# Performance work log

Hardware: AMD Instinct MI355X
Metric: run time of the kernel (lower is better)

The kernel has to match this reference:

```python
import jax, jax.numpy as jnp
import numpy as np

D_MODEL = 512
NHEAD = 8
D_K = D_MODEL // NHEAD


def setup_inputs() -> dict:
    key = jax.random.key(0)
    ks = jax.random.split(key, 9)
    s = 1.0 / np.sqrt(D_MODEL)
    x = jax.random.normal(ks[0], (2, 2048, D_MODEL), dtype=jnp.float32)
    # torch Linear weights: [out_features, in_features]
    Wq = jax.random.uniform(ks[1], (D_MODEL, D_MODEL), jnp.float32, -s, s)
    bq = jax.random.uniform(ks[2], (D_MODEL,), jnp.float32, -s, s)
    Wk = jax.random.uniform(ks[3], (D_MODEL, D_MODEL), jnp.float32, -s, s)
    bk = jax.random.uniform(ks[4], (D_MODEL,), jnp.float32, -s, s)
    Wv = jax.random.uniform(ks[5], (D_MODEL, D_MODEL), jnp.float32, -s, s)
    bv = jax.random.uniform(ks[6], (D_MODEL,), jnp.float32, -s, s)
    Wo = jax.random.uniform(ks[7], (D_MODEL, D_MODEL), jnp.float32, -s, s)
    bo = jax.random.uniform(ks[8], (D_MODEL,), jnp.float32, -s, s)
    return {"x": x, "Wq": Wq, "bq": bq, "Wk": Wk, "bk": bk,
            "Wv": Wv, "bv": bv, "Wo": Wo, "bo": bo}


def reference(x, Wq, bq, Wk, bk, Wv, bv, Wo, bo):
    B, S, D = x.shape
    H, Dk = NHEAD, D_K

    def proj(W, b):
        # torch Linear: x @ W.T + b -> [B, S, D] -> [B, H, S, Dk]
        y = jnp.einsum('bsd,ed->bse', x, W) + b
        return y.reshape(B, S, H, Dk).transpose(0, 2, 1, 3)

    q = proj(Wq, bq)
    k = proj(Wk, bk)
    v = proj(Wv, bv)

    scores = jnp.einsum('bhqd,bhkd->bhqk', q, k) / jnp.sqrt(jnp.float32(Dk))
    attn = jax.nn.softmax(scores, axis=-1)  # explicit O(S^2) attention matrix
    out = jnp.einsum('bhqk,bhkd->bhqd', attn, v)
    out = out.transpose(0, 2, 1, 3).reshape(B, S, D)
    return jnp.einsum('bsd,ed->bse', out, Wo) + bo
```

## Files before the change

### kernel.cpp

```cpp
#include <hip/hip_runtime.h>

typedef __bf16 bf16_t;
typedef bf16_t bf16x8 __attribute__((ext_vector_type(8)));
typedef bf16_t bf16x4 __attribute__((ext_vector_type(4)));
typedef float  floatx4 __attribute__((ext_vector_type(4)));
typedef short  s16x4   __attribute__((ext_vector_type(4)));

#define D_MODEL 512
#define NHEAD   8
#define DK      64
#define BATCH   2
#define SEQ     2048
#define MTOT    (BATCH*SEQ)
#define QSCALE  0.18033688011112042591f

static __device__ __forceinline__ floatx4 mfma16(bf16x8 a, bf16x8 b, floatx4 c) {
    return __builtin_amdgcn_mfma_f32_16x16x32_bf16(a, b, c, 0, 0, 0);
}
static __device__ __forceinline__ floatx4 mfma16k16(s16x4 a, s16x4 b, floatx4 c) {
    return __builtin_amdgcn_mfma_f32_16x16x16bf16_1k(a, b, c, 0, 0, 0);
}

static __device__ __forceinline__ void glds16(bf16_t* lds, const bf16_t* g) {
    __builtin_amdgcn_global_load_lds(
        (const __attribute__((address_space(1))) unsigned int*)g,
        (__attribute__((address_space(3))) unsigned int*)lds,
        16, 0, 0);
}

__global__ __launch_bounds__(256)
void to_bf16(const float* __restrict__ x,
             const float* __restrict__ Wq, const float* __restrict__ Wk,
             const float* __restrict__ Wv, const float* __restrict__ Wo,
             bf16_t* __restrict__ xb, bf16_t* __restrict__ wqb,
             bf16_t* __restrict__ wkb, bf16_t* __restrict__ wvb,
             bf16_t* __restrict__ wob)
{
    const int blk = blockIdx.x;
    const float* src; bf16_t* dst; size_t base;
    if      (blk < 1024) { src = x;  dst = xb;  base = (size_t)blk * 2048; }
    else if (blk < 1152) { src = Wq; dst = wqb; base = (size_t)(blk - 1024) * 2048; }
    else if (blk < 1280) { src = Wk; dst = wkb; base = (size_t)(blk - 1152) * 2048; }
    else if (blk < 1408) { src = Wv; dst = wvb; base = (size_t)(blk - 1280) * 2048; }
    else                 { src = Wo; dst = wob; base = (size_t)(blk - 1408) * 2048; }
    const size_t off = base + (size_t)threadIdx.x * 8;
    const float4 a = *(const float4*)(src + off);
    const float4 b = *(const float4*)(src + off + 4);
    bf16x8 p;
    p[0]=(bf16_t)a.x; p[1]=(bf16_t)a.y; p[2]=(bf16_t)a.z; p[3]=(bf16_t)a.w;
    p[4]=(bf16_t)b.x; p[5]=(bf16_t)b.y; p[6]=(bf16_t)b.z; p[7]=(bf16_t)b.w;
    const size_t off2 = off ^ ((((off >> 10) & 3)) << 3);
    *(bf16x8*)(dst + off2) = p;
}

__global__ __launch_bounds__(256)
void qkv_proj(const bf16_t* __restrict__ xb,
              const bf16_t* __restrict__ wqb, const float* __restrict__ bq,
              const bf16_t* __restrict__ wkb, const float* __restrict__ bk,
              const bf16_t* __restrict__ wvb, const float* __restrict__ bv,
              bf16_t* __restrict__ q_ws, bf16_t* __restrict__ k_ws,
              bf16_t* __restrict__ vt_ws)
{
    __shared__ bf16_t As[128 * 32];
    __shared__ bf16_t Bs[128 * 32];

    const int mtile = blockIdx.x;
    const int ntile = blockIdx.y;
    const int which = ntile >> 2;
    const int nsub  = ntile & 3;
    const bf16_t* W   = (which == 0) ? wqb : (which == 1) ? wkb : wvb;
    const float* bias = (which == 0) ? bq  : (which == 1) ? bk  : bv;

    const int tid  = threadIdx.x;
    const int lane = tid & 63;
    const int wave = tid >> 6;
    const int wm = wave & 1, wn = wave >> 1;
    const int l15 = lane & 15, quad = lane >> 4;
    const int m0 = mtile * 128;
    const int n0 = nsub * 128;
    const int lr = lane >> 2;
    const int lc = (lane & 3) * 8;
    const int csw = (quad ^ ((l15 >> 1) & 3)) * 8;

    floatx4 acc[4][4] = {};

    for (int k0 = 0; k0 < 512; k0 += 32) {
        __syncthreads();
        #pragma unroll
        for (int q = 0; q < 2; ++q) {
            const int r = wave * 32 + q * 16;
            glds16(&As[r * 32], xb + (size_t)(m0 + r + lr) * 512 + k0 + lc);
            glds16(&Bs[r * 32], W  + (size_t)(n0 + r + lr) * 512 + k0 + lc);
        }
        __syncthreads();

        bf16x8 af[4], bfr[4];
        #pragma unroll
        for (int i = 0; i < 4; ++i)
            af[i] = *(const bf16x8*)(&As[(wm * 64 + i * 16 + l15) * 32 + csw]);
        #pragma unroll
        for (int j = 0; j < 4; ++j)
            bfr[j] = *(const bf16x8*)(&Bs[(wn * 64 + j * 16 + l15) * 32 + csw]);
        #pragma unroll
        for (int i = 0; i < 4; ++i)
            #pragma unroll
            for (int j = 0; j < 4; ++j)
                acc[i][j] = mfma16(af[i], bfr[j], acc[i][j]);
    }

    #pragma unroll
    for (int j = 0; j < 4; ++j) {
        const int e = n0 + wn * 64 + j * 16 + l15;
        const float be = bias[e];
        const int h = e >> 6, d = e & 63;
        #pragma unroll
        for (int i = 0; i < 4; ++i) {
            const int mbase = m0 + wm * 64 + i * 16 + quad * 4;
            const int b = mbase >> 11;
            const int sl = mbase & 2047;
            floatx4 c = acc[i][j];
            if (which == 2) {
                bf16x4 pk;
                #pragma unroll
                for (int r = 0; r < 4; ++r) pk[r] = (bf16_t)(c[r] + be);
                const int slz = (sl & ~63) | ((((sl >> 3) & 7) ^ (d & 7)) << 3) | (sl & 7);
                *(bf16x4*)(vt_ws + ((size_t)((b * 8 + h) * 64 + d)) * 2048 + slz) = pk;
            } else if (which == 1) {
                #pragma unroll
                for (int r = 0; r < 4; ++r) {
                    const int s = sl + r;
                    const int dz = ((((d >> 3) ^ (s & 7))) << 3) | (d & 7);
                    k_ws[(size_t)(b * 8 + h) * (SEQ * DK) + (size_t)s * 64 + dz] =
                        (bf16_t)(c[r] + be);
                }
            } else {
                #pragma unroll
                for (int r = 0; r < 4; ++r)
                    q_ws[(size_t)(b * 8 + h) * (SEQ * DK) + (size_t)(sl + r) * 64 + d] =
                        (bf16_t)((c[r] + be) * QSCALE);
            }
        }
    }
}

__global__ __launch_bounds__(256, 4)
void attn_kernel(const bf16_t* __restrict__ q_ws, const bf16_t* __restrict__ k_ws,
                 const bf16_t* __restrict__ vt_ws, bf16_t* __restrict__ attn_ws)
{
    __shared__ bf16_t Kt[2][64 * 64];
    __shared__ bf16_t Vt[2][64 * 64];

    const int bh = blockIdx.x;
    const int qt = blockIdx.y;
    const int tid = threadIdx.x, lane = tid & 63, wave = tid >> 6;
    const int l15 = lane & 15, quad = lane >> 4;
    const int g  = wave >> 1;
    const int wq = wave & 1;

    const bf16_t* Qb  = q_ws  + (size_t)bh * SEQ * DK;
    const bf16_t* Kb  = k_ws  + (size_t)bh * SEQ * DK;
    const bf16_t* Vtb = vt_ws + (size_t)bh * DK * SEQ;

    const int sp = wave & 1;
    bf16_t* stile = (wave < 2) ? &Kt[sp][0] : &Vt[sp][0];
    const int srow8 = lane >> 3;
    const int scol  = (lane & 7) * 8;

    bf16x8 aq[2][2];
    #pragma unroll
    for (int mt = 0; mt < 2; ++mt)
        #pragma unroll
        for (int c = 0; c < 2; ++c)
            aq[mt][c] = *(const bf16x8*)(Qb +
                (size_t)(qt * 64 + wq * 32 + mt * 16 + l15) * 64 + c * 32 + quad * 8);

    floatx4 O[2][4] = {};
    float rs[2] = {0.f, 0.f};
    const int ksw0 = ((0 + quad) ^ (l15 & 7)) * 8;
    const int ksw1 = ((4 + quad) ^ (l15 & 7)) * 8;

    for (int t = 0; t < 16; ++t) {
        __syncthreads();
        {
            const int kg = t * 128 + sp * 64;
            if (wave < 2) {
                #pragma unroll
                for (int i = 0; i < 8; ++i)
                    glds16(stile + i * 512,
                           Kb + (size_t)(kg + i * 8 + srow8) * 64 + scol);
            } else {
                #pragma unroll
                for (int i = 0; i < 8; ++i)
                    glds16(stile + i * 512,
                           Vtb + (size_t)(i * 8 + srow8) * 2048 + kg + scol);
            }
        }
        __syncthreads();

        s16x4 pf[2][4];
        #pragma unroll
        for (int kf = 0; kf < 4; ++kf) {
            const bf16_t* krow = &Kt[g][(kf * 16 + l15) * 64];
            bf16x8 k0 = *(const bf16x8*)(krow + ksw0);
            bf16x8 k1 = *(const bf16x8*)(krow + ksw1);
            #pragma unroll
            for (int mt = 0; mt < 2; ++mt) {
                floatx4 z = {0.f, 0.f, 0.f, 0.f};
                z = mfma16(k0, aq[mt][0], z);
                z = mfma16(k1, aq[mt][1], z);
                bf16x4 pk;
                float s = 0.f;
                #pragma unroll
                for (int r = 0; r < 4; ++r) {
                    const float p = __builtin_amdgcn_exp2f(z[r]);
                    s += p;
                    pk[r] = (bf16_t)p;
                }
                rs[mt] += s;
                pf[mt][kf] = __builtin_bit_cast(s16x4, pk);
            }
        }

        #pragma unroll
        for (int kg = 0; kg < 4; ++kg) {
            const int voff = (((kg * 2 + (quad >> 1)) ^ (l15 & 7)) * 8) + (quad & 1) * 4;
            #pragma unroll
            for (int df = 0; df < 4; ++df) {
                const s16x4 v = *(const s16x4*)(&Vt[g][(df * 16 + l15) * 64 + voff]);
                #pragma unroll
                for (int mt = 0; mt < 2; ++mt)
                    O[mt][df] = mfma16k16(pf[mt][kg], v, O[mt][df]);
            }
        }
    }

    #pragma unroll
    for (int mt = 0; mt < 2; ++mt) {
        rs[mt] += __shfl_xor(rs[mt], 16, 64);
        rs[mt] += __shfl_xor(rs[mt], 32, 64);
    }

    float* scratch = (float*)&Kt[0][0];
    __syncthreads();
    if (g == 1) {
        float* s = scratch + (size_t)(wq * 64 + lane) * 35;
        #pragma unroll
        for (int mt = 0; mt < 2; ++mt) {
            #pragma unroll
            for (int df = 0; df < 4; ++df)
                #pragma unroll
                for (int r = 0; r < 4; ++r) s[mt * 16 + df * 4 + r] = O[mt][df][r];
            s[32 + mt] = rs[mt];
        }
    }
    __syncthreads();
    if (g == 0) {
        const float* s = scratch + (size_t)(wq * 64 + lane) * 35;
        #pragma unroll
        for (int mt = 0; mt < 2; ++mt) {
            #pragma unroll
            for (int df = 0; df < 4; ++df)
                #pragma unroll
                for (int r = 0; r < 4; ++r) O[mt][df][r] += s[mt * 16 + df * 4 + r];
            rs[mt] += s[32 + mt];
        }

        const int b = bh >> 3, h = bh & 7;
        #pragma unroll
        for (int mt = 0; mt < 2; ++mt)
            #pragma unroll
            for (int r = 0; r < 4; ++r) {
                const float rv = __shfl(rs[mt], (quad << 4) + ((quad & 3) << 2) + r, 64);
                const float rinv = 1.0f / rv;
                const int s_ = qt * 64 + wq * 32 + mt * 16 + quad * 4 + r;
                const int sw = ((s_ >> 1) & 3) << 3;
                const size_t base = ((size_t)b * 2048 + s_) * 512;
                #pragma unroll
                for (int df = 0; df < 4; ++df) {
                    const int col = h * 64 + df * 16 + l15;
                    attn_ws[base + (col ^ sw)] = (bf16_t)(O[mt][df][r] * rinv);
                }
            }
    }
}

__global__ __launch_bounds__(256)
void out_proj(const bf16_t* __restrict__ attn_ws, const bf16_t* __restrict__ wob,
              const float* __restrict__ bo, float* __restrict__ y)
{
    __shared__ bf16_t As[64 * 32];
    __shared__ bf16_t Bs[128 * 32];

    const int mtile = blockIdx.x;
    const int ntile = blockIdx.y;
    const int tid = threadIdx.x, lane = tid & 63, wave = tid >> 6;
    const int wm = wave & 1, wn = wave >> 1;
    const int l15 = lane & 15, quad = lane >> 4;
    const int m0 = mtile * 64;
    const int n0 = ntile * 128;
    const int lr = lane >> 2, lc = (lane & 3) * 8;
    const int csw = (quad ^ ((l15 >> 1) & 3)) * 8;

    floatx4 acc[2][4] = {};

    for (int k0 = 0; k0 < 512; k0 += 32) {
        __syncthreads();
        glds16(&As[wave * 16 * 32], attn_ws + (size_t)(m0 + wave * 16 + lr) * 512 + k0 + lc);
        #pragma unroll
        for (int q = 0; q < 2; ++q) {
            const int r = wave * 32 + q * 16;
            glds16(&Bs[r * 32], wob + (size_t)(n0 + r + lr) * 512 + k0 + lc);
        }
        __syncthreads();

        bf16x8 af[2], bfr[4];
        #pragma unroll
        for (int i = 0; i < 2; ++i)
            af[i] = *(const bf16x8*)(&As[(wm * 32 + i * 16 + l15) * 32 + csw]);
        #pragma unroll
        for (int j = 0; j < 4; ++j)
            bfr[j] = *(const bf16x8*)(&Bs[(wn * 64 + j * 16 + l15) * 32 + csw]);
        #pragma unroll
        for (int i = 0; i < 2; ++i)
            #pragma unroll
            for (int j = 0; j < 4; ++j)
                acc[i][j] = mfma16(af[i], bfr[j], acc[i][j]);
    }

    #pragma unroll
    for (int j = 0; j < 4; ++j) {
        const int e = n0 + wn * 64 + j * 16 + l15;
        const float be = bo[e];
        #pragma unroll
        for (int i = 0; i < 2; ++i) {
            const int mb = m0 + wm * 32 + i * 16 + quad * 4;
            #pragma unroll
            for (int r = 0; r < 4; ++r)
                y[(size_t)(mb + r) * 512 + e] = acc[i][j][r] + be;
        }
    }
}

extern "C" void kernel_launch(void* const* d_in, const int* in_sizes, int n_in,
                              void* d_out, int out_size, void* d_ws, size_t ws_size,
                              hipStream_t stream) {
    (void)in_sizes; (void)n_in; (void)out_size; (void)ws_size;
    const float* x  = (const float*)d_in[0];
    const float* Wq = (const float*)d_in[1];
    const float* bq = (const float*)d_in[2];
    const float* Wk = (const float*)d_in[3];
    const float* bk = (const float*)d_in[4];
    const float* Wv = (const float*)d_in[5];
    const float* bv = (const float*)d_in[6];
    const float* Wo = (const float*)d_in[7];
    const float* bo = (const float*)d_in[8];

    bf16_t* xb   = (bf16_t*)d_ws;
    bf16_t* wqb  = xb   + (size_t)MTOT * D_MODEL;
    bf16_t* wkb  = wqb  + (size_t)D_MODEL * D_MODEL;
    bf16_t* wvb  = wkb  + (size_t)D_MODEL * D_MODEL;
    bf16_t* wob  = wvb  + (size_t)D_MODEL * D_MODEL;
    bf16_t* qws  = wob  + (size_t)D_MODEL * D_MODEL;
    bf16_t* kws  = qws  + (size_t)MTOT * D_MODEL;
    bf16_t* vtws = kws  + (size_t)MTOT * D_MODEL;
    bf16_t* aws  = vtws + (size_t)MTOT * D_MODEL;

    to_bf16    <<<1536, 256, 0, stream>>>(x, Wq, Wk, Wv, Wo, xb, wqb, wkb, wvb, wob);
    qkv_proj   <<<dim3(32, 12), 256, 0, stream>>>(xb, wqb, bq, wkb, bk, wvb, bv, qws, kws, vtws);
    attn_kernel<<<dim3(16, 32), 256, 0, stream>>>(qws, kws, vtws, aws);
    out_proj   <<<dim3(64, 4),  256, 0, stream>>>(aws, wob, bo, (float*)d_out);
}
```

Measured before the change: 131.8 us.

## Halve QKV projection M-tile and widen attention blocks to eight waves

The QKV projection now uses 64-row M tiles, doubling its grid to give more blocks across the GPU's compute units. The attention kernel moves to 512 threads with four key-split wave groups, each loading its own 64-key K/V slice, so the outer loop runs 8 iterations instead of 16. A two-stage LDS reduction merges the four partial O and row-sum sets. This trades more LDS use (64 KiB per block) and an extra reduction step for more parallelism per query tile, but it may lower occupancy.

Measured after the change: 130.1 us. No clear change (-1.3%).

```diff
diff --git a/kernel.cpp b/kernel.cpp
--- a/kernel.cpp
+++ b/kernel.cpp
@@ -61,7 +61,7 @@
               bf16_t* __restrict__ q_ws, bf16_t* __restrict__ k_ws,
               bf16_t* __restrict__ vt_ws)
 {
-    __shared__ bf16_t As[128 * 32];
+    __shared__ bf16_t As[64 * 32];
     __shared__ bf16_t Bs[128 * 32];
 
     const int mtile = blockIdx.x;
@@ -76,33 +76,33 @@
     const int wave = tid >> 6;
     const int wm = wave & 1, wn = wave >> 1;
     const int l15 = lane & 15, quad = lane >> 4;
-    const int m0 = mtile * 128;
+    const int m0 = mtile * 64;
     const int n0 = nsub * 128;
     const int lr = lane >> 2;
     const int lc = (lane & 3) * 8;
     const int csw = (quad ^ ((l15 >> 1) & 3)) * 8;
 
-    floatx4 acc[4][4] = {};
+    floatx4 acc[2][4] = {};
 
     for (int k0 = 0; k0 < 512; k0 += 32) {
         __syncthreads();
+        glds16(&As[wave * 16 * 32], xb + (size_t)(m0 + wave * 16 + lr) * 512 + k0 + lc);
         #pragma unroll
         for (int q = 0; q < 2; ++q) {
             const int r = wave * 32 + q * 16;
-            glds16(&As[r * 32], xb + (size_t)(m0 + r + lr) * 512 + k0 + lc);
-            glds16(&Bs[r * 32], W  + (size_t)(n0 + r + lr) * 512 + k0 + lc);
-        }
-        __syncthreads();
-
-        bf16x8 af[4], bfr[4];
-        #pragma unroll
-        for (int i = 0; i < 4; ++i)
-            af[i] = *(const bf16x8*)(&As[(wm * 64 + i * 16 + l15) * 32 + csw]);
+            glds16(&Bs[r * 32], W + (size_t)(n0 + r + lr) * 512 + k0 + lc);
+        }
+        __syncthreads();
+
+        bf16x8 af[2], bfr[4];
+        #pragma unroll
+        for (int i = 0; i < 2; ++i)
+            af[i] = *(const bf16x8*)(&As[(wm * 32 + i * 16 + l15) * 32 + csw]);
         #pragma unroll
         for (int j = 0; j < 4; ++j)
             bfr[j] = *(const bf16x8*)(&Bs[(wn * 64 + j * 16 + l15) * 32 + csw]);
         #pragma unroll
-        for (int i = 0; i < 4; ++i)
+        for (int i = 0; i < 2; ++i)
             #pragma unroll
             for (int j = 0; j < 4; ++j)
                 acc[i][j] = mfma16(af[i], bfr[j], acc[i][j]);
@@ -114,8 +114,8 @@
         const float be = bias[e];
         const int h = e >> 6, d = e & 63;
         #pragma unroll
-        for (int i = 0; i < 4; ++i) {
-            const int mbase = m0 + wm * 64 + i * 16 + quad * 4;
+        for (int i = 0; i < 2; ++i) {
+            const int mbase = m0 + wm * 32 + i * 16 + quad * 4;
             const int b = mbase >> 11;
             const int sl = mbase & 2047;
             floatx4 c = acc[i][j];
@@ -143,26 +143,26 @@
     }
 }
 
-__global__ __launch_bounds__(256, 4)
+__global__ __launch_bounds__(512, 4)
 void attn_kernel(const bf16_t* __restrict__ q_ws, const bf16_t* __restrict__ k_ws,
                  const bf16_t* __restrict__ vt_ws, bf16_t* __restrict__ attn_ws)
 {
-    __shared__ bf16_t Kt[2][64 * 64];
-    __shared__ bf16_t Vt[2][64 * 64];
+    __shared__ bf16_t Kt[4][64 * 64];
+    __shared__ bf16_t Vt[4][64 * 64];
 
     const int bh = blockIdx.x;
     const int qt = blockIdx.y;
     const int tid = threadIdx.x, lane = tid & 63, wave = tid >> 6;
     const int l15 = lane & 15, quad = lane >> 4;
-    const int g  = wave >> 1;
-    const int wq = wave & 1;
+    const int g  = wave & 3;
+    const int wq = wave >> 2;
 
     const bf16_t* Qb  = q_ws  + (size_t)bh * SEQ * DK;
     const bf16_t* Kb  = k_ws  + (size_t)bh * SEQ * DK;
     const bf16_t* Vtb = vt_ws + (size_t)bh * DK * SEQ;
 
-    const int sp = wave & 1;
-    bf16_t* stile = (wave < 2) ? &Kt[sp][0] : &Vt[sp][0];
+    const int sp = wave & 3;
+    bf16_t* stile = (wave < 4) ? &Kt[sp][0] : &Vt[sp][0];
     const int srow8 = lane >> 3;
     const int scol  = (lane & 7) * 8;
 
@@ -179,11 +179,11 @@
     const int ksw0 = ((0 + quad) ^ (l15 & 7)) * 8;
     const int ksw1 = ((4 + quad) ^ (l15 & 7)) * 8;
 
-    for (int t = 0; t < 16; ++t) {
+    for (int t = 0; t < 8; ++t) {
         __syncthreads();
         {
-            const int kg = t * 128 + sp * 64;
-            if (wave < 2) {
+            const int kg = t * 256 + sp * 64;
+            if (wave < 4) {
                 #pragma unroll
                 for (int i = 0; i < 8; ++i)
                     glds16(stile + i * 512,
@@ -222,14 +222,14 @@
         }
 
         #pragma unroll
-        for (int kg = 0; kg < 4; ++kg) {
-            const int voff = (((kg * 2 + (quad >> 1)) ^ (l15 & 7)) * 8) + (quad & 1) * 4;
+        for (int kg2 = 0; kg2 < 4; ++kg2) {
+            const int voff = (((kg2 * 2 + (quad >> 1)) ^ (l15 & 7)) * 8) + (quad & 1) * 4;
             #pragma unroll
             for (int df = 0; df < 4; ++df) {
                 const s16x4 v = *(const s16x4*)(&Vt[g][(df * 16 + l15) * 64 + voff]);
                 #pragma unroll
                 for (int mt = 0; mt < 2; ++mt)
-                    O[mt][df] = mfma16k16(pf[mt][kg], v, O[mt][df]);
+                    O[mt][df] = mfma16k16(pf[mt][kg2], v, O[mt][df]);
             }
         }
     }
@@ -241,6 +241,30 @@
     }
 
     float* scratch = (float*)&Kt[0][0];
+    __syncthreads();
+    if (g >= 2) {
+        float* s = scratch + (size_t)((wq * 2 + (g - 2)) * 64 + lane) * 35;
+        #pragma unroll
+        for (int mt = 0; mt < 2; ++mt) {
+            #pragma unroll
+            for (int df = 0; df < 4; ++df)
+                #pragma unroll
+                for (int r = 0; r < 4; ++r) s[mt * 16 + df * 4 + r] = O[mt][df][r];
+            s[32 + mt] = rs[mt];
+        }
+    }
+    __syncthreads();
+    if (g < 2) {
+        const float* s = scratch + (size_t)((wq * 2 + g) * 64 + lane) * 35;
+        #pragma unroll
+        for (int mt = 0; mt < 2; ++mt) {
+            #pragma unroll
+            for (int df = 0; df < 4; ++df)
+                #pragma unroll
+                for (int r = 0; r < 4; ++r) O[mt][df][r] += s[mt * 16 + df * 4 + r];
+            rs[mt] += s[32 + mt];
+        }
+    }
     __syncthreads();
     if (g == 1) {
         float* s = scratch + (size_t)(wq * 64 + lane) * 35;
@@ -366,7 +390,7 @@
     bf16_t* aws  = vtws + (size_t)MTOT * D_MODEL;
 
     to_bf16    <<<1536, 256, 0, stream>>>(x, Wq, Wk, Wv, Wo, xb, wqb, wkb, wvb, wob);
-    qkv_proj   <<<dim3(32, 12), 256, 0, stream>>>(xb, wqb, bq, wkb, bk, wvb, bv, qws, kws, vtws);
-    attn_kernel<<<dim3(16, 32), 256, 0, stream>>>(qws, kws, vtws, aws);
+    qkv_proj   <<<dim3(64, 12), 256, 0, stream>>>(xb, wqb, bq, wkb, bk, wvb, bv, qws, kws, vtws);
+    attn_kernel<<<dim3(16, 32), 512, 0, stream>>>(qws, kws, vtws, aws);
     out_proj   <<<dim3(64, 4),  256, 0, stream>>>(aws, wob, bo, (float*)d_out);
 }
```
